# Kernel optimization log

Measured on AMD Instinct MI355X. Metric: run time of the kernel, lower is better.

Reference implementation:

```python
import jax, jax.numpy as jnp
import numpy as np

M_BLEND = 0.3
LR_REFINE = 0.1
N_REFINE = 10
N_SAMPLES = 256
USE_INFONCE = True
MARGIN = 0.2
TAU = 0.07


def safe_norm(x, eps=1e-8):
    return x / jnp.maximum(jnp.linalg.norm(x, axis=-1, keepdims=True), eps)


def setup_inputs() -> dict:
    key = jax.random.key(0)
    k1, k2, k3, k4 = jax.random.split(key, 4)
    fg_proto = safe_norm(jax.random.normal(k1, (64, 512), dtype=jnp.float32))
    bg_proto = safe_norm(jax.random.normal(k2, (64, 512), dtype=jnp.float32))
    F_map = jax.random.normal(k3, (16, 512, 96, 96), dtype=jnp.float32)
    M_map = jax.random.uniform(k4, (16, 96, 96), dtype=jnp.float32)
    return {"fg_proto": fg_proto, "bg_proto": bg_proto, "F_map": F_map, "M_map": M_map}


def _refine(feats, protos):
    # iterative k-means-like refinement: argmax assign -> per-cluster mean -> blended, renormalized centroid
    p = protos
    K = p.shape[0]
    ones = jnp.ones((feats.shape[0],), feats.dtype)
    for it in range(N_REFINE):
        step = LR_REFINE / (1.0 + 0.5 * it)
        assign = jnp.argmax(feats @ p.T, axis=1)                      # [S]
        sums = jax.ops.segment_sum(feats, assign, num_segments=K)    # [K, C]
        counts = jax.ops.segment_sum(ones, assign, num_segments=K)   # [K]
        cluster_mean = sums / jnp.maximum(counts, 1.0)[:, None]
        new_p = safe_norm((1.0 - step) * p + step * cluster_mean)
        p = jnp.where((counts > 0)[:, None], new_p, p)                # only update non-empty clusters
    return p


def reference(fg_proto, bg_proto, F_map, M_map):
    N, C, H, W = F_map.shape
    # M_map already at (H, W): nearest interpolation is identity; clamp to [0, 1]
    M_flat = jnp.clip(M_map.reshape(-1), 0.0, 1.0)                    # [N*H*W]
    F_flat = safe_norm(F_map.transpose(0, 2, 3, 1).reshape(-1, C))    # [N*H*W, C]

    sim_fg = F_flat @ fg_proto.T                                      # [P, Kf]
    sim_bg = F_flat @ bg_proto.T                                      # [P, Kb]
    dist_fg_min = 1.0 - sim_fg.max(axis=1)
    dist_bg_min = 1.0 - sim_bg.max(axis=1)

    k = min(N_SAMPLES, F_flat.shape[0])
    score_fg = jax.lax.stop_gradient(dist_fg_min * M_flat)
    score_bg = jax.lax.stop_gradient(dist_bg_min * (1.0 - M_flat))
    pos_idx = jax.lax.top_k(score_fg, k)[1]
    neg_idx = jax.lax.top_k(score_bg, k)[1]

    # refinement runs under no_grad in the original
    F_sg = jax.lax.stop_gradient(F_flat)
    p_fg = _refine(F_sg[pos_idx], jax.lax.stop_gradient(fg_proto))
    p_bg = _refine(F_sg[neg_idx], jax.lax.stop_gradient(bg_proto))

    # triplet loss (note: sim_neg also uses p_fg, as in the original)
    pos_feats = safe_norm(F_flat[pos_idx])
    neg_feats = safe_norm(F_flat[neg_idx])
    sim_pos = (pos_feats @ p_fg.T).max(axis=1).mean()
    sim_neg = (neg_feats @ p_fg.T).max(axis=1).mean()
    loss = jax.nn.relu(MARGIN + sim_neg - sim_pos)

    if USE_INFONCE:
        pos_sim = pos_feats @ p_fg.T / TAU                            # [k, Kf]
        neg_sim = pos_feats @ p_bg.T / TAU                            # [k, Kb]
        numerator = jax.scipy.special.logsumexp(pos_sim, axis=1)
        denominator = jax.scipy.special.logsumexp(jnp.concatenate([pos_sim, neg_sim], axis=1), axis=1)
        loss = loss + 0.25 * (-(numerator - denominator).mean())

    refined_fg = safe_norm((1.0 - M_BLEND) * fg_proto + M_BLEND * p_fg)
    refined_bg = safe_norm((1.0 - M_BLEND) * bg_proto + M_BLEND * p_bg)
    return loss, refined_fg, refined_bg
```

## Files before the change

### kernel.cpp

```cpp
#include <hip/hip_runtime.h>
#include <math.h>

#define P_TOTAL 147456
#define HW 9216
#define CHW (512*9216)
#define C_DIM 512
#define KP 64

__device__ __forceinline__ unsigned f2key(float f) {
    unsigned u = __float_as_uint(f);
    return (u & 0x80000000u) ? ~u : (u | 0x80000000u);
}

__global__ void k_init(const float* __restrict__ fg, const float* __restrict__ bg,
                       float* __restrict__ protoT, float* __restrict__ pwork) {
    int i = blockIdx.x * 256 + threadIdx.x;
    int side = i >> 15;
    int r = i & 32767;
    int k = r >> 9;
    int c = r & 511;
    float v = (side ? bg : fg)[k * 512 + c];
    protoT[side * 32768 + c * 64 + k] = v;
    pwork[side * 32768 + k * 512 + c] = v;
}

__global__ __launch_bounds__(256) void k_score(const float* __restrict__ F,
                                               const float* __restrict__ protoT,
                                               float* __restrict__ md_fg,
                                               float* __restrict__ md_bg,
                                               float* __restrict__ n2out) {
    __shared__ float lds[2048];
    const int side = blockIdx.y;
    const int p = blockIdx.x * 256 + threadIdx.x;
    const int n = p / HW;
    const int hw = p - n * HW;
    const float* Fp = F + (size_t)n * CHW + hw;
    const float* PT = protoT + side * (C_DIM * 64);

    float acc[64];
#pragma unroll
    for (int k = 0; k < 64; ++k) acc[k] = 0.f;
    float n2 = 0.f;

    for (int cc = 0; cc < 16; ++cc) {
        __syncthreads();
#pragma unroll
        for (int i = 0; i < 8; ++i)
            lds[threadIdx.x + 256 * i] = PT[cc * 2048 + threadIdx.x + 256 * i];
        __syncthreads();
        for (int c = 0; c < 32; ++c) {
            float f = Fp[(size_t)(cc * 32 + c) * HW];
            if (side == 0) n2 = fmaf(f, f, n2);
#pragma unroll
            for (int k = 0; k < 64; ++k) acc[k] = fmaf(f, lds[c * 64 + k], acc[k]);
        }
    }
    float m = acc[0];
#pragma unroll
    for (int k = 1; k < 64; ++k) m = fmaxf(m, acc[k]);
    if (side == 0) { md_fg[p] = m; n2out[p] = n2; }
    else          { md_bg[p] = m; }
}

__global__ void k_combine(const float* __restrict__ M,
                          float* __restrict__ sfg, float* __restrict__ sbg,
                          float* __restrict__ n2inv) {
    int p = blockIdx.x * 256 + threadIdx.x;
    float inv = 1.f / fmaxf(sqrtf(n2inv[p]), 1e-8f);
    float m = fminf(fmaxf(M[p], 0.f), 1.f);
    float sf = (1.f - sfg[p] * inv) * m;
    float sb = (1.f - sbg[p] * inv) * (1.f - m);
    sfg[p] = sf; sbg[p] = sb; n2inv[p] = inv;
}

__global__ void k_hist1(const float* __restrict__ sfg, const float* __restrict__ sbg,
                        unsigned* __restrict__ hist) {
    int side = blockIdx.y;
    int p = blockIdx.x * 256 + threadIdx.x;
    float s = side ? sbg[p] : sfg[p];
    atomicAdd(&hist[side * 65536 + (f2key(s) >> 16)], 1u);
}

__global__ void k_hist2(const float* __restrict__ sfg, const float* __restrict__ sbg,
                        const int* __restrict__ ctrl, unsigned* __restrict__ hist2) {
    int side = blockIdx.y;
    int p = blockIdx.x * 256 + threadIdx.x;
    float s = side ? sbg[p] : sfg[p];
    unsigned key = f2key(s);
    if ((int)(key >> 16) == ctrl[side * 8 + 0])
        atomicAdd(&hist2[side * 65536 + (key & 0xffffu)], 1u);
}

__global__ __launch_bounds__(1024) void k_scan(const unsigned* __restrict__ hist,
                                               int* __restrict__ ctrl, int pass) {
    __shared__ unsigned sd[1024];
    int side = blockIdx.x;
    const unsigned* h = hist + side * 65536;
    int t = threadIdx.x;
    unsigned partial = 0;
    for (int j = 0; j < 64; ++j) partial += h[65535 - (t * 64 + j)];
    sd[t] = partial;
    __syncthreads();
    for (int off = 1; off < 1024; off <<= 1) {
        unsigned v = (t >= off) ? sd[t - off] : 0u;
        __syncthreads();
        sd[t] += v;
        __syncthreads();
    }
    unsigned incl = sd[t];
    unsigned excl = incl - partial;
    unsigned target = (pass == 0) ? 256u : (unsigned)ctrl[side * 8 + 1];
    if (excl < target && target <= incl) {
        unsigned cum = excl;
        for (int j = 0; j < 64; ++j) {
            int b = 65535 - (t * 64 + j);
            unsigned c = h[b];
            if (cum + c >= target) {
                if (pass == 0) {
                    ctrl[side * 8 + 0] = b;
                    ctrl[side * 8 + 1] = (int)(target - cum);
                } else {
                    unsigned vkey = ((unsigned)ctrl[side * 8 + 0] << 16) | (unsigned)b;
                    ctrl[side * 8 + 2] = (int)vkey;
                    int n_gt = (int)(256u - (unsigned)ctrl[side * 8 + 1] + cum);
                    ctrl[side * 8 + 3] = n_gt;
                    ctrl[side * 8 + 4] = 256 - n_gt;
                }
                break;
            }
            cum += c;
        }
    }
}

__global__ void k_collect(const float* __restrict__ sfg, const float* __restrict__ sbg,
                          int* __restrict__ ctrl, int* __restrict__ idx, int* __restrict__ ties) {
    int side = blockIdx.y;
    int p = blockIdx.x * 256 + threadIdx.x;
    float s = side ? sbg[p] : sfg[p];
    unsigned key = f2key(s);
    unsigned vkey = (unsigned)ctrl[side * 8 + 2];
    if (key > vkey) {
        int pos = atomicAdd(&ctrl[side * 8 + 5], 1);
        idx[side * 256 + pos] = p;
    } else if (key == vkey) {
        int pos = atomicAdd(&ctrl[side * 8 + 6], 1);
        if (pos < 512) ties[side * 512 + pos] = p;
    }
}

__global__ void k_finalize(int* __restrict__ ctrl, int* __restrict__ idx, int* __restrict__ ties) {
    int side = threadIdx.x;
    if (side >= 2) return;
    int n_gt = ctrl[side * 8 + 3];
    int need = ctrl[side * 8 + 4];
    int cnt = ctrl[side * 8 + 6];
    if (cnt > 512) cnt = 512;
    int* tb = ties + side * 512;
    for (int q = 0; q < need; ++q) {
        int mi = q;
        for (int j = q + 1; j < cnt; ++j) if (tb[j] < tb[mi]) mi = j;
        int tmp = tb[q]; tb[q] = tb[mi]; tb[mi] = tmp;
        idx[side * 256 + n_gt + q] = tb[q];
    }
}

__global__ void k_gather(const float* __restrict__ F, const float* __restrict__ inv,
                         const int* __restrict__ idx, float* __restrict__ feats) {
    int b = blockIdx.x;
    int side = b >> 8, j = b & 255;
    int p = idx[side * 256 + j];
    float iv = inv[p];
    int n = p / HW, hw = p - n * HW;
    const float* Fp = F + (size_t)n * CHW + hw;
    float* o = feats + (size_t)(side * 256 + j) * 512;
    for (int c = threadIdx.x; c < 512; c += 256)
        o[c] = Fp[(size_t)c * HW] * iv;
}

__global__ __launch_bounds__(256) void k_assign(const float* __restrict__ feats,
                                                const float* __restrict__ pwork,
                                                float* __restrict__ sums,
                                                float* __restrict__ counts) {
    int w = blockIdx.x * 4 + (threadIdx.x >> 6);
    int lane = threadIdx.x & 63;
    int side = w >> 8, j = w & 255;
    const float4* fr = (const float4*)(feats + (size_t)(side * 256 + j) * 512);
    const float4* pw = (const float4*)(pwork + (size_t)side * 32768 + (size_t)lane * 512);
    float dot = 0.f;
#pragma unroll 4
    for (int c = 0; c < 128; ++c) {
        float4 a = fr[c], b = pw[c];
        dot = fmaf(a.x, b.x, dot); dot = fmaf(a.y, b.y, dot);
        dot = fmaf(a.z, b.z, dot); dot = fmaf(a.w, b.w, dot);
    }
    float bv = dot; int bi = lane;
#pragma unroll
    for (int m = 32; m >= 1; m >>= 1) {
        float ov = __shfl_xor(bv, m);
        int oi = __shfl_xor(bi, m);
        if (ov > bv || (ov == bv && oi < bi)) { bv = ov; bi = oi; }
    }
    if (lane == 0) atomicAdd(&counts[side * 64 + bi], 1.f);
    const float* frf = feats + (size_t)(side * 256 + j) * 512;
    float* srow = sums + (size_t)side * 32768 + (size_t)bi * 512;
#pragma unroll
    for (int i = 0; i < 8; ++i) {
        int c = lane + i * 64;
        atomicAdd(&srow[c], frf[c]);
    }
}

__global__ __launch_bounds__(64) void k_update(float* __restrict__ pwork,
                                               float* __restrict__ sums,
                                               float* __restrict__ counts,
                                               float step) {
    int side = blockIdx.x >> 6, k = blockIdx.x & 63;
    int lane = threadIdx.x;
    float cnt = counts[side * 64 + k];
    float* srow = sums + (size_t)side * 32768 + (size_t)k * 512;
    float* prow = pwork + (size_t)side * 32768 + (size_t)k * 512;
    float bl[8]; float n2 = 0.f;
#pragma unroll
    for (int i = 0; i < 8; ++i) {
        int c = lane + i * 64;
        float mean = srow[c] / fmaxf(cnt, 1.f);
        float v = (1.f - step) * prow[c] + step * mean;
        bl[i] = v; n2 = fmaf(v, v, n2);
        srow[c] = 0.f;
    }
#pragma unroll
    for (int m = 32; m >= 1; m >>= 1) n2 += __shfl_xor(n2, m);
    float inv = 1.f / fmaxf(sqrtf(n2), 1e-8f);
    if (cnt > 0.f) {
#pragma unroll
        for (int i = 0; i < 8; ++i) prow[lane + i * 64] = bl[i] * inv;
    }
    if (lane == 0) counts[side * 64 + k] = 0.f;
}

__global__ __launch_bounds__(256) void k_losspart(const float* __restrict__ feats,
                                                  const float* __restrict__ pwork,
                                                  float* __restrict__ lpart) {
    int w = blockIdx.x * 4 + (threadIdx.x >> 6);
    int lane = threadIdx.x & 63;
    int half = w >> 8, j = w & 255;
    const float4* fr = (const float4*)(feats + (size_t)(half * 256 + j) * 512);
    const float4* pf = (const float4*)(pwork + (size_t)lane * 512);
    const float4* pb = (const float4*)(pwork + 32768 + (size_t)lane * 512);
    if (half == 0) {
        float d1 = 0.f, d2 = 0.f;
        for (int c = 0; c < 128; ++c) {
            float4 a = fr[c], x = pf[c], y = pb[c];
            d1 = fmaf(a.x, x.x, d1); d1 = fmaf(a.y, x.y, d1);
            d1 = fmaf(a.z, x.z, d1); d1 = fmaf(a.w, x.w, d1);
            d2 = fmaf(a.x, y.x, d2); d2 = fmaf(a.y, y.y, d2);
            d2 = fmaf(a.z, y.z, d2); d2 = fmaf(a.w, y.w, d2);
        }
        float smax = d1;
        for (int m = 32; m >= 1; m >>= 1) smax = fmaxf(smax, __shfl_xor(smax, m));
        float a = d1 / 0.07f, b = d2 / 0.07f;
        float m1 = a;
        for (int m = 32; m >= 1; m >>= 1) m1 = fmaxf(m1, __shfl_xor(m1, m));
        float mb = b;
        for (int m = 32; m >= 1; m >>= 1) mb = fmaxf(mb, __shfl_xor(mb, m));
        float md = fmaxf(m1, mb);
        float sn = expf(a - m1);
        for (int m = 32; m >= 1; m >>= 1) sn += __shfl_xor(sn, m);
        float sdn = expf(a - md) + expf(b - md);
        for (int m = 32; m >= 1; m >>= 1) sdn += __shfl_xor(sdn, m);
        float num = m1 + logf(sn);
        float den = md + logf(sdn);
        if (lane == 0) { lpart[j] = smax; lpart[512 + j] = num - den; }
    } else {
        float d1 = 0.f;
        for (int c = 0; c < 128; ++c) {
            float4 a = fr[c], x = pf[c];
            d1 = fmaf(a.x, x.x, d1); d1 = fmaf(a.y, x.y, d1);
            d1 = fmaf(a.z, x.z, d1); d1 = fmaf(a.w, x.w, d1);
        }
        float smax = d1;
        for (int m = 32; m >= 1; m >>= 1) smax = fmaxf(smax, __shfl_xor(smax, m));
        if (lane == 0) lpart[256 + j] = smax;
    }
}

__global__ __launch_bounds__(256) void k_final(const float* __restrict__ lpart,
                                               float* __restrict__ out) {
    __shared__ float red[3][4];
    int t = threadIdx.x;
    float sp = lpart[t], sn = lpart[256 + t], nm = lpart[512 + t];
    for (int m = 32; m >= 1; m >>= 1) {
        sp += __shfl_xor(sp, m); sn += __shfl_xor(sn, m); nm += __shfl_xor(nm, m);
    }
    int wv = t >> 6;
    if ((t & 63) == 0) { red[0][wv] = sp; red[1][wv] = sn; red[2][wv] = nm; }
    __syncthreads();
    if (t == 0) {
        float SP = 0, SN = 0, NM = 0;
        for (int i = 0; i < 4; ++i) { SP += red[0][i]; SN += red[1][i]; NM += red[2][i]; }
        SP /= 256.f; SN /= 256.f; NM /= 256.f;
        out[0] = fmaxf(0.f, 0.2f + SN - SP) + 0.25f * (-NM);
    }
}

__global__ __launch_bounds__(64) void k_refined(const float* __restrict__ fg,
                                                const float* __restrict__ bg,
                                                const float* __restrict__ pwork,
                                                float* __restrict__ out) {
    int side = blockIdx.x >> 6, k = blockIdx.x & 63;
    int lane = threadIdx.x;
    const float* proto = (side ? bg : fg) + (size_t)k * 512;
    const float* prow = pwork + (size_t)side * 32768 + (size_t)k * 512;
    float bl[8]; float n2 = 0.f;
#pragma unroll
    for (int i = 0; i < 8; ++i) {
        int c = lane + i * 64;
        float v = 0.7f * proto[c] + 0.3f * prow[c];
        bl[i] = v; n2 = fmaf(v, v, n2);
    }
#pragma unroll
    for (int m = 32; m >= 1; m >>= 1) n2 += __shfl_xor(n2, m);
    float inv = 1.f / fmaxf(sqrtf(n2), 1e-8f);
    float* o = out + 1 + (size_t)side * 32768 + (size_t)k * 512;
#pragma unroll
    for (int i = 0; i < 8; ++i) o[lane + i * 64] = bl[i] * inv;
}

extern "C" void kernel_launch(void* const* d_in, const int* in_sizes, int n_in,
                              void* d_out, int out_size, void* d_ws, size_t ws_size,
                              hipStream_t stream) {
    const float* fg = (const float*)d_in[0];
    const float* bg = (const float*)d_in[1];
    const float* F  = (const float*)d_in[2];
    const float* M  = (const float*)d_in[3];
    float* out = (float*)d_out;
    char* ws = (char*)d_ws;

    size_t o = 0;
    auto alloc = [&](size_t bytes) { size_t r = o; o += (bytes + 1023) & ~(size_t)1023; return r; };
    size_t off_hist1 = alloc(2 * 65536 * 4);
    size_t off_hist2 = alloc(2 * 65536 * 4);
    size_t off_ctrl  = alloc(64);
    size_t off_cnts  = alloc(2 * 64 * 4);
    size_t off_sums  = alloc(2 * 64 * 512 * 4);
    size_t zbytes = o;
    size_t off_sfg   = alloc(P_TOTAL * 4);
    size_t off_sbg   = alloc(P_TOTAL * 4);
    size_t off_n2    = alloc(P_TOTAL * 4);
    size_t off_pT    = alloc(2 * 512 * 64 * 4);
    size_t off_idx   = alloc(2 * 256 * 4);
    size_t off_ties  = alloc(2 * 512 * 4);
    size_t off_feats = alloc(2 * 256 * 512 * 4);
    size_t off_pwork = alloc(2 * 64 * 512 * 4);
    size_t off_lpart = alloc(768 * 4);

    unsigned* hist1 = (unsigned*)(ws + off_hist1);
    unsigned* hist2 = (unsigned*)(ws + off_hist2);
    int* ctrl   = (int*)(ws + off_ctrl);
    float* cnts = (float*)(ws + off_cnts);
    float* sums = (float*)(ws + off_sums);
    float* sfg  = (float*)(ws + off_sfg);
    float* sbg  = (float*)(ws + off_sbg);
    float* n2   = (float*)(ws + off_n2);
    float* pT   = (float*)(ws + off_pT);
    int* idx    = (int*)(ws + off_idx);
    int* ties   = (int*)(ws + off_ties);
    float* feats = (float*)(ws + off_feats);
    float* pwork = (float*)(ws + off_pwork);
    float* lpart = (float*)(ws + off_lpart);

    hipMemsetAsync(ws, 0, zbytes, stream);
    k_init<<<256, 256, 0, stream>>>(fg, bg, pT, pwork);
    k_score<<<dim3(576, 2), 256, 0, stream>>>(F, pT, sfg, sbg, n2);
    k_combine<<<576, 256, 0, stream>>>(M, sfg, sbg, n2);
    k_hist1<<<dim3(576, 2), 256, 0, stream>>>(sfg, sbg, hist1);
    k_scan<<<2, 1024, 0, stream>>>(hist1, ctrl, 0);
    k_hist2<<<dim3(576, 2), 256, 0, stream>>>(sfg, sbg, ctrl, hist2);
    k_scan<<<2, 1024, 0, stream>>>(hist2, ctrl, 1);
    k_collect<<<dim3(576, 2), 256, 0, stream>>>(sfg, sbg, ctrl, idx, ties);
    k_finalize<<<1, 64, 0, stream>>>(ctrl, idx, ties);
    k_gather<<<512, 256, 0, stream>>>(F, n2, idx, feats);
    for (int it = 0; it < 10; ++it) {
        k_assign<<<128, 256, 0, stream>>>(feats, pwork, sums, cnts);
        k_update<<<128, 64, 0, stream>>>(pwork, sums, cnts, (float)(0.1 / (1.0 + 0.5 * it)));
    }
    k_losspart<<<128, 256, 0, stream>>>(feats, pwork, lpart);
    k_final<<<1, 256, 0, stream>>>(lpart, out);
    k_refined<<<128, 64, 0, stream>>>(fg, bg, pwork, out);
}
```

Baseline: 1.139 ms.

## Fuse fg/bg scoring into one pass with 4x32 register tiling

The scoring kernel now handles both prototype sets in a single launch, so F is read once instead of twice. Each thread computes a 4-pixel by 32-prototype register tile, with the four wavefront groups splitting the 128 fg+bg prototypes. Prototype columns are read from shared memory as float4, and the per-half maxima are combined through shared memory at the end. The point is to cut global traffic on F and raise FMA-to-load reuse. In exchange it uses a larger LDS footprint, 128 accumulator registers per thread, and a launch bound of 2 blocks per SM that may cause spills.

```diff
diff --git a/kernel.cpp b/kernel.cpp
--- a/kernel.cpp
+++ b/kernel.cpp
@@ -20,46 +20,100 @@
     int k = r >> 9;
     int c = r & 511;
     float v = (side ? bg : fg)[k * 512 + c];
-    protoT[side * 32768 + c * 64 + k] = v;
+    protoT[c * 128 + side * 64 + k] = v;
     pwork[side * 32768 + k * 512 + c] = v;
 }
 
-__global__ __launch_bounds__(256) void k_score(const float* __restrict__ F,
-                                               const float* __restrict__ protoT,
-                                               float* __restrict__ md_fg,
-                                               float* __restrict__ md_bg,
-                                               float* __restrict__ n2out) {
-    __shared__ float lds[2048];
-    const int side = blockIdx.y;
-    const int p = blockIdx.x * 256 + threadIdx.x;
-    const int n = p / HW;
-    const int hw = p - n * HW;
-    const float* Fp = F + (size_t)n * CHW + hw;
-    const float* PT = protoT + side * (C_DIM * 64);
-
-    float acc[64];
-#pragma unroll
-    for (int k = 0; k < 64; ++k) acc[k] = 0.f;
-    float n2 = 0.f;
-
-    for (int cc = 0; cc < 16; ++cc) {
+__global__ __launch_bounds__(256, 2) void k_score(const float* __restrict__ F,
+                                                  const float* __restrict__ protoT,
+                                                  float* __restrict__ md_fg,
+                                                  float* __restrict__ md_bg,
+                                                  float* __restrict__ n2out) {
+    __shared__ float lds[64 * 128];
+    const int t = threadIdx.x;
+    const int lane = t & 63;
+    const int g = t >> 6;
+    const int p0 = blockIdx.x * 256 + lane;
+    const int n = p0 / HW;
+    const int hw0 = p0 - n * HW;
+    const float* Fp = F + (size_t)n * CHW + hw0;
+
+    float acc[32][4];
+#pragma unroll
+    for (int i = 0; i < 32; ++i)
+#pragma unroll
+        for (int pt = 0; pt < 4; ++pt) acc[i][pt] = 0.f;
+    float nn[4] = {0.f, 0.f, 0.f, 0.f};
+
+    for (int chunk = 0; chunk < 8; ++chunk) {
         __syncthreads();
-#pragma unroll
-        for (int i = 0; i < 8; ++i)
-            lds[threadIdx.x + 256 * i] = PT[cc * 2048 + threadIdx.x + 256 * i];
+        {
+            const float4* src = (const float4*)(protoT + chunk * 8192);
+            float4* dst = (float4*)lds;
+#pragma unroll
+            for (int i = 0; i < 8; ++i) dst[t + 256 * i] = src[t + 256 * i];
+        }
         __syncthreads();
-        for (int c = 0; c < 32; ++c) {
-            float f = Fp[(size_t)(cc * 32 + c) * HW];
-            if (side == 0) n2 = fmaf(f, f, n2);
-#pragma unroll
-            for (int k = 0; k < 64; ++k) acc[k] = fmaf(f, lds[c * 64 + k], acc[k]);
-        }
-    }
-    float m = acc[0];
-#pragma unroll
-    for (int k = 1; k < 64; ++k) m = fmaxf(m, acc[k]);
-    if (side == 0) { md_fg[p] = m; n2out[p] = n2; }
-    else          { md_bg[p] = m; }
+#pragma unroll 4
+        for (int c = 0; c < 64; ++c) {
+            const float* Fc = Fp + (size_t)(chunk * 64 + c) * HW;
+            float f0 = Fc[0];
+            float f1 = Fc[64];
+            float f2 = Fc[128];
+            float f3 = Fc[192];
+            if (g == 0) {
+                nn[0] = fmaf(f0, f0, nn[0]);
+                nn[1] = fmaf(f1, f1, nn[1]);
+                nn[2] = fmaf(f2, f2, nn[2]);
+                nn[3] = fmaf(f3, f3, nn[3]);
+            }
+            const float4* pv = (const float4*)(lds + c * 128 + g * 32);
+#pragma unroll
+            for (int i = 0; i < 8; ++i) {
+                float4 b = pv[i];
+                acc[i * 4 + 0][0] = fmaf(f0, b.x, acc[i * 4 + 0][0]);
+                acc[i * 4 + 0][1] = fmaf(f1, b.x, acc[i * 4 + 0][1]);
+                acc[i * 4 + 0][2] = fmaf(f2, b.x, acc[i * 4 + 0][2]);
+                acc[i * 4 + 0][3] = fmaf(f3, b.x, acc[i * 4 + 0][3]);
+                acc[i * 4 + 1][0] = fmaf(f0, b.y, acc[i * 4 + 1][0]);
+                acc[i * 4 + 1][1] = fmaf(f1, b.y, acc[i * 4 + 1][1]);
+                acc[i * 4 + 1][2] = fmaf(f2, b.y, acc[i * 4 + 1][2]);
+                acc[i * 4 + 1][3] = fmaf(f3, b.y, acc[i * 4 + 1][3]);
+                acc[i * 4 + 2][0] = fmaf(f0, b.z, acc[i * 4 + 2][0]);
+                acc[i * 4 + 2][1] = fmaf(f1, b.z, acc[i * 4 + 2][1]);
+                acc[i * 4 + 2][2] = fmaf(f2, b.z, acc[i * 4 + 2][2]);
+                acc[i * 4 + 2][3] = fmaf(f3, b.z, acc[i * 4 + 2][3]);
+                acc[i * 4 + 3][0] = fmaf(f0, b.w, acc[i * 4 + 3][0]);
+                acc[i * 4 + 3][1] = fmaf(f1, b.w, acc[i * 4 + 3][1]);
+                acc[i * 4 + 3][2] = fmaf(f2, b.w, acc[i * 4 + 3][2]);
+                acc[i * 4 + 3][3] = fmaf(f3, b.w, acc[i * 4 + 3][3]);
+            }
+        }
+    }
+
+    float m[4];
+#pragma unroll
+    for (int pt = 0; pt < 4; ++pt) {
+        float mm = acc[0][pt];
+#pragma unroll
+        for (int i = 1; i < 32; ++i) mm = fmaxf(mm, acc[i][pt]);
+        m[pt] = mm;
+    }
+    __syncthreads();
+#pragma unroll
+    for (int pt = 0; pt < 4; ++pt) lds[(g * 4 + pt) * 64 + lane] = m[pt];
+    __syncthreads();
+    if (g == 0) {
+#pragma unroll
+        for (int pt = 0; pt < 4; ++pt) {
+            md_fg[p0 + pt * 64] = fmaxf(lds[(0 + pt) * 64 + lane], lds[(4 + pt) * 64 + lane]);
+            n2out[p0 + pt * 64] = nn[pt];
+        }
+    } else if (g == 2) {
+#pragma unroll
+        for (int pt = 0; pt < 4; ++pt)
+            md_bg[p0 + pt * 64] = fmaxf(lds[(8 + pt) * 64 + lane], lds[(12 + pt) * 64 + lane]);
+    }
 }
 
 __global__ void k_combine(const float* __restrict__ M,
@@ -348,7 +402,7 @@
     size_t off_sfg   = alloc(P_TOTAL * 4);
     size_t off_sbg   = alloc(P_TOTAL * 4);
     size_t off_n2    = alloc(P_TOTAL * 4);
-    size_t off_pT    = alloc(2 * 512 * 64 * 4);
+    size_t off_pT    = alloc(512 * 128 * 4);
     size_t off_idx   = alloc(2 * 256 * 4);
     size_t off_ties  = alloc(2 * 512 * 4);
     size_t off_feats = alloc(2 * 256 * 512 * 4);
@@ -372,7 +426,7 @@
 
     hipMemsetAsync(ws, 0, zbytes, stream);
     k_init<<<256, 256, 0, stream>>>(fg, bg, pT, pwork);
-    k_score<<<dim3(576, 2), 256, 0, stream>>>(F, pT, sfg, sbg, n2);
+    k_score<<<576, 256, 0, stream>>>(F, pT, sfg, sbg, n2);
     k_combine<<<576, 256, 0, stream>>>(M, sfg, sbg, n2);
     k_hist1<<<dim3(576, 2), 256, 0, stream>>>(sfg, sbg, hist1);
     k_scan<<<2, 1024, 0, stream>>>(hist1, ctrl, 0);
```

Result: no change. 1.144 ms (+0.5%).

## Register-tile score GEMM over fg+bg jointly and fuse combine and histogram

Applied to the files above, without the earlier changes.

Rewrites the scoring kernel so each block handles 576 pixels against both fg and bg prototypes at once. Each wave owns 16 prototypes and each thread holds 9 pixels in registers, with the next channel's loads issued ahead of use. The old design read F twice (once per side) with one pixel per thread. The score combine and first-pass histogram are folded into the same kernel's epilogue. The assign kernel now reads a transposed prototype copy that update keeps in sync, which adds extra strided writes per iteration. Using 256 blocks with launch_bounds(512,1) and 144 accumulators per thread risks low occupancy or register spills.

```diff
diff --git a/kernel.cpp b/kernel.cpp
--- a/kernel.cpp
+++ b/kernel.cpp
@@ -4,8 +4,6 @@
 #define P_TOTAL 147456
 #define HW 9216
 #define CHW (512*9216)
-#define C_DIM 512
-#define KP 64
 
 __device__ __forceinline__ unsigned f2key(float f) {
     unsigned u = __float_as_uint(f);
@@ -13,82 +11,122 @@
 }
 
 __global__ void k_init(const float* __restrict__ fg, const float* __restrict__ bg,
-                       float* __restrict__ protoT, float* __restrict__ pwork) {
+                       float* __restrict__ protoT, float* __restrict__ pwork,
+                       float* __restrict__ pwT) {
     int i = blockIdx.x * 256 + threadIdx.x;
     int side = i >> 15;
     int r = i & 32767;
     int k = r >> 9;
     int c = r & 511;
     float v = (side ? bg : fg)[k * 512 + c];
-    protoT[side * 32768 + c * 64 + k] = v;
+    protoT[c * 128 + side * 64 + k] = v;
     pwork[side * 32768 + k * 512 + c] = v;
-}
-
-__global__ __launch_bounds__(256) void k_score(const float* __restrict__ F,
-                                               const float* __restrict__ protoT,
-                                               float* __restrict__ md_fg,
-                                               float* __restrict__ md_bg,
-                                               float* __restrict__ n2out) {
-    __shared__ float lds[2048];
-    const int side = blockIdx.y;
-    const int p = blockIdx.x * 256 + threadIdx.x;
-    const int n = p / HW;
-    const int hw = p - n * HW;
-    const float* Fp = F + (size_t)n * CHW + hw;
-    const float* PT = protoT + side * (C_DIM * 64);
-
-    float acc[64];
-#pragma unroll
-    for (int k = 0; k < 64; ++k) acc[k] = 0.f;
-    float n2 = 0.f;
-
-    for (int cc = 0; cc < 16; ++cc) {
+    pwT[side * 32768 + c * 64 + k] = v;
+}
+
+__global__ __launch_bounds__(512, 1) void k_score(const float* __restrict__ F,
+                                                  const float* __restrict__ protoT,
+                                                  const float* __restrict__ M,
+                                                  float* __restrict__ sfg,
+                                                  float* __restrict__ sbg,
+                                                  float* __restrict__ invout,
+                                                  unsigned* __restrict__ hist) {
+    __shared__ float lds[8192];
+    const int t = threadIdx.x;
+    const int lane = t & 63;
+    const int w = t >> 6;
+    const int p0 = blockIdx.x * 576 + lane;
+    const int n = p0 / HW;
+    const int hw0 = p0 - n * HW;
+    const float* Fb = F + (size_t)n * CHW;
+
+    float acc[16][9];
+#pragma unroll
+    for (int jj = 0; jj < 16; ++jj)
+#pragma unroll
+        for (int i = 0; i < 9; ++i) acc[jj][i] = 0.f;
+    float nn[9];
+#pragma unroll
+    for (int i = 0; i < 9; ++i) nn[i] = 0.f;
+
+    auto ldch = [&](float (&dst)[9], int ch) {
+        int chc = ch > 511 ? 511 : ch;
+        const float* q = Fb + hw0 + (size_t)chc * HW;
+#pragma unroll
+        for (int i = 0; i < 9; ++i) dst[i] = q[i * 64];
+    };
+    auto kstep = [&](const float (&f)[9], int cc) {
+        const float4* pv4 = (const float4*)(lds + cc * 128 + w * 16);
+#pragma unroll
+        for (int j4 = 0; j4 < 4; ++j4) {
+            float4 bq = pv4[j4];
+#pragma unroll
+            for (int i = 0; i < 9; ++i) {
+                acc[j4 * 4 + 0][i] = fmaf(f[i], bq.x, acc[j4 * 4 + 0][i]);
+                acc[j4 * 4 + 1][i] = fmaf(f[i], bq.y, acc[j4 * 4 + 1][i]);
+                acc[j4 * 4 + 2][i] = fmaf(f[i], bq.z, acc[j4 * 4 + 2][i]);
+                acc[j4 * 4 + 3][i] = fmaf(f[i], bq.w, acc[j4 * 4 + 3][i]);
+            }
+        }
+    };
+
+    float fa[9], fb[9];
+    ldch(fa, 0); ldch(fb, 1);
+    int ch = 2;
+
+    for (int chunk = 0; chunk < 8; ++chunk) {
         __syncthreads();
-#pragma unroll
-        for (int i = 0; i < 8; ++i)
-            lds[threadIdx.x + 256 * i] = PT[cc * 2048 + threadIdx.x + 256 * i];
+        {
+            const float4* src = (const float4*)(protoT + chunk * 8192);
+            float4* dst = (float4*)lds;
+#pragma unroll
+            for (int i2 = 0; i2 < 4; ++i2) dst[t + 512 * i2] = src[t + 512 * i2];
+        }
         __syncthreads();
-        for (int c = 0; c < 32; ++c) {
-            float f = Fp[(size_t)(cc * 32 + c) * HW];
-            if (side == 0) n2 = fmaf(f, f, n2);
-#pragma unroll
-            for (int k = 0; k < 64; ++k) acc[k] = fmaf(f, lds[c * 64 + k], acc[k]);
-        }
-    }
-    float m = acc[0];
-#pragma unroll
-    for (int k = 1; k < 64; ++k) m = fmaxf(m, acc[k]);
-    if (side == 0) { md_fg[p] = m; n2out[p] = n2; }
-    else          { md_bg[p] = m; }
-}
-
-__global__ void k_combine(const float* __restrict__ M,
-                          float* __restrict__ sfg, float* __restrict__ sbg,
-                          float* __restrict__ n2inv) {
-    int p = blockIdx.x * 256 + threadIdx.x;
-    float inv = 1.f / fmaxf(sqrtf(n2inv[p]), 1e-8f);
-    float m = fminf(fmaxf(M[p], 0.f), 1.f);
-    float sf = (1.f - sfg[p] * inv) * m;
-    float sb = (1.f - sbg[p] * inv) * (1.f - m);
-    sfg[p] = sf; sbg[p] = sb; n2inv[p] = inv;
-}
-
-__global__ void k_hist1(const float* __restrict__ sfg, const float* __restrict__ sbg,
-                        unsigned* __restrict__ hist) {
-    int side = blockIdx.y;
-    int p = blockIdx.x * 256 + threadIdx.x;
-    float s = side ? sbg[p] : sfg[p];
-    atomicAdd(&hist[side * 65536 + (f2key(s) >> 16)], 1u);
-}
-
-__global__ void k_hist2(const float* __restrict__ sfg, const float* __restrict__ sbg,
-                        const int* __restrict__ ctrl, unsigned* __restrict__ hist2) {
-    int side = blockIdx.y;
-    int p = blockIdx.x * 256 + threadIdx.x;
-    float s = side ? sbg[p] : sfg[p];
-    unsigned key = f2key(s);
-    if ((int)(key >> 16) == ctrl[side * 8 + 0])
-        atomicAdd(&hist2[side * 65536 + (key & 0xffffu)], 1u);
+        for (int c2 = 0; c2 < 32; ++c2) {
+            if (w == 0) {
+#pragma unroll
+                for (int i = 0; i < 9; ++i) nn[i] = fmaf(fa[i], fa[i], nn[i]);
+            }
+            kstep(fa, c2 * 2);
+            ldch(fa, ch++);
+            if (w == 0) {
+#pragma unroll
+                for (int i = 0; i < 9; ++i) nn[i] = fmaf(fb[i], fb[i], nn[i]);
+            }
+            kstep(fb, c2 * 2 + 1);
+            ldch(fb, ch++);
+        }
+    }
+
+    float m16[9];
+#pragma unroll
+    for (int i = 0; i < 9; ++i) {
+        float mm = acc[0][i];
+#pragma unroll
+        for (int jj = 1; jj < 16; ++jj) mm = fmaxf(mm, acc[jj][i]);
+        m16[i] = mm;
+    }
+    __syncthreads();
+#pragma unroll
+    for (int i = 0; i < 9; ++i) lds[w * 576 + i * 64 + lane] = m16[i];
+    if (w == 0) {
+#pragma unroll
+        for (int i = 0; i < 9; ++i) lds[4608 + i * 64 + lane] = nn[i];
+    }
+    __syncthreads();
+    for (int pi = t; pi < 576; pi += 512) {
+        int p = blockIdx.x * 576 + pi;
+        float fgm = fmaxf(fmaxf(lds[pi], lds[576 + pi]), fmaxf(lds[1152 + pi], lds[1728 + pi]));
+        float bgm = fmaxf(fmaxf(lds[2304 + pi], lds[2880 + pi]), fmaxf(lds[3456 + pi], lds[4032 + pi]));
+        float inv = 1.f / fmaxf(sqrtf(lds[4608 + pi]), 1e-8f);
+        float mm = fminf(fmaxf(M[p], 0.f), 1.f);
+        float sf = (1.f - fgm * inv) * mm;
+        float sb = (1.f - bgm * inv) * (1.f - mm);
+        sfg[p] = sf; sbg[p] = sb; invout[p] = inv;
+        atomicAdd(&hist[f2key(sf) >> 16], 1u);
+        atomicAdd(&hist[65536 + (f2key(sb) >> 16)], 1u);
+    }
 }
 
 __global__ __launch_bounds__(1024) void k_scan(const unsigned* __restrict__ hist,
@@ -133,6 +171,16 @@
     }
 }
 
+__global__ void k_hist2(const float* __restrict__ sfg, const float* __restrict__ sbg,
+                        const int* __restrict__ ctrl, unsigned* __restrict__ hist2) {
+    int side = blockIdx.y;
+    int p = blockIdx.x * 256 + threadIdx.x;
+    float s = side ? sbg[p] : sfg[p];
+    unsigned key = f2key(s);
+    if ((int)(key >> 16) == ctrl[side * 8 + 0])
+        atomicAdd(&hist2[side * 65536 + (key & 0xffffu)], 1u);
+}
+
 __global__ void k_collect(const float* __restrict__ sfg, const float* __restrict__ sbg,
                           int* __restrict__ ctrl, int* __restrict__ idx, int* __restrict__ ties) {
     int side = blockIdx.y;
@@ -179,21 +227,18 @@
 }
 
 __global__ __launch_bounds__(256) void k_assign(const float* __restrict__ feats,
-                                                const float* __restrict__ pwork,
+                                                const float* __restrict__ pwT,
                                                 float* __restrict__ sums,
                                                 float* __restrict__ counts) {
     int w = blockIdx.x * 4 + (threadIdx.x >> 6);
     int lane = threadIdx.x & 63;
     int side = w >> 8, j = w & 255;
-    const float4* fr = (const float4*)(feats + (size_t)(side * 256 + j) * 512);
-    const float4* pw = (const float4*)(pwork + (size_t)side * 32768 + (size_t)lane * 512);
+    const float* fr = feats + (size_t)(side * 256 + j) * 512;
+    const float* pT = pwT + (size_t)side * 32768;
     float dot = 0.f;
-#pragma unroll 4
-    for (int c = 0; c < 128; ++c) {
-        float4 a = fr[c], b = pw[c];
-        dot = fmaf(a.x, b.x, dot); dot = fmaf(a.y, b.y, dot);
-        dot = fmaf(a.z, b.z, dot); dot = fmaf(a.w, b.w, dot);
-    }
+#pragma unroll 8
+    for (int c = 0; c < 512; ++c)
+        dot = fmaf(fr[c], pT[c * 64 + lane], dot);
     float bv = dot; int bi = lane;
 #pragma unroll
     for (int m = 32; m >= 1; m >>= 1) {
@@ -202,16 +247,16 @@
         if (ov > bv || (ov == bv && oi < bi)) { bv = ov; bi = oi; }
     }
     if (lane == 0) atomicAdd(&counts[side * 64 + bi], 1.f);
-    const float* frf = feats + (size_t)(side * 256 + j) * 512;
     float* srow = sums + (size_t)side * 32768 + (size_t)bi * 512;
 #pragma unroll
     for (int i = 0; i < 8; ++i) {
         int c = lane + i * 64;
-        atomicAdd(&srow[c], frf[c]);
+        atomicAdd(&srow[c], fr[c]);
     }
 }
 
 __global__ __launch_bounds__(64) void k_update(float* __restrict__ pwork,
+                                               float* __restrict__ pwT,
                                                float* __restrict__ sums,
                                                float* __restrict__ counts,
                                                float step) {
@@ -220,6 +265,7 @@
     float cnt = counts[side * 64 + k];
     float* srow = sums + (size_t)side * 32768 + (size_t)k * 512;
     float* prow = pwork + (size_t)side * 32768 + (size_t)k * 512;
+    float* pT = pwT + (size_t)side * 32768;
     float bl[8]; float n2 = 0.f;
 #pragma unroll
     for (int i = 0; i < 8; ++i) {
@@ -234,7 +280,12 @@
     float inv = 1.f / fmaxf(sqrtf(n2), 1e-8f);
     if (cnt > 0.f) {
 #pragma unroll
-        for (int i = 0; i < 8; ++i) prow[lane + i * 64] = bl[i] * inv;
+        for (int i = 0; i < 8; ++i) {
+            int c = lane + i * 64;
+            float v = bl[i] * inv;
+            prow[c] = v;
+            pT[(size_t)c * 64 + k] = v;
+        }
     }
     if (lane == 0) counts[side * 64 + k] = 0.f;
 }
@@ -347,12 +398,13 @@
     size_t zbytes = o;
     size_t off_sfg   = alloc(P_TOTAL * 4);
     size_t off_sbg   = alloc(P_TOTAL * 4);
-    size_t off_n2    = alloc(P_TOTAL * 4);
-    size_t off_pT    = alloc(2 * 512 * 64 * 4);
+    size_t off_inv   = alloc(P_TOTAL * 4);
+    size_t off_pT    = alloc(512 * 128 * 4);
+    size_t off_pwork = alloc(2 * 64 * 512 * 4);
+    size_t off_pwT   = alloc(2 * 512 * 64 * 4);
     size_t off_idx   = alloc(2 * 256 * 4);
     size_t off_ties  = alloc(2 * 512 * 4);
-    size_t off_feats = alloc(2 * 256 * 512 * 4);
-    size_t off_pwork = alloc(2 * 64 * 512 * 4);
+    size_t off_feats = alloc(512 * 512 * 4);
     size_t off_lpart = alloc(768 * 4);
 
     unsigned* hist1 = (unsigned*)(ws + off_hist1);
@@ -362,28 +414,27 @@
     float* sums = (float*)(ws + off_sums);
     float* sfg  = (float*)(ws + off_sfg);
     float* sbg  = (float*)(ws + off_sbg);
-    float* n2   = (float*)(ws + off_n2);
+    float* inv  = (float*)(ws + off_inv);
     float* pT   = (float*)(ws + off_pT);
+    float* pwork = (float*)(ws + off_pwork);
+    float* pwT  = (float*)(ws + off_pwT);
     int* idx    = (int*)(ws + off_idx);
     int* ties   = (int*)(ws + off_ties);
     float* feats = (float*)(ws + off_feats);
-    float* pwork = (float*)(ws + off_pwork);
     float* lpart = (float*)(ws + off_lpart);
 
     hipMemsetAsync(ws, 0, zbytes, stream);
-    k_init<<<256, 256, 0, stream>>>(fg, bg, pT, pwork);
-    k_score<<<dim3(576, 2), 256, 0, stream>>>(F, pT, sfg, sbg, n2);
-    k_combine<<<576, 256, 0, stream>>>(M, sfg, sbg, n2);
-    k_hist1<<<dim3(576, 2), 256, 0, stream>>>(sfg, sbg, hist1);
+    k_init<<<256, 256, 0, stream>>>(fg, bg, pT, pwork, pwT);
+    k_score<<<256, 512, 0, stream>>>(F, pT, M, sfg, sbg, inv, hist1);
     k_scan<<<2, 1024, 0, stream>>>(hist1, ctrl, 0);
     k_hist2<<<dim3(576, 2), 256, 0, stream>>>(sfg, sbg, ctrl, hist2);
     k_scan<<<2, 1024, 0, stream>>>(hist2, ctrl, 1);
     k_collect<<<dim3(576, 2), 256, 0, stream>>>(sfg, sbg, ctrl, idx, ties);
     k_finalize<<<1, 64, 0, stream>>>(ctrl, idx, ties);
-    k_gather<<<512, 256, 0, stream>>>(F, n2, idx, feats);
+    k_gather<<<512, 256, 0, stream>>>(F, inv, idx, feats);
     for (int it = 0; it < 10; ++it) {
-        k_assign<<<128, 256, 0, stream>>>(feats, pwork, sums, cnts);
-        k_update<<<128, 64, 0, stream>>>(pwork, sums, cnts, (float)(0.1 / (1.0 + 0.5 * it)));
+        k_assign<<<128, 256, 0, stream>>>(feats, pwT, sums, cnts);
+        k_update<<<128, 64, 0, stream>>>(pwork, pwT, sums, cnts, (float)(0.1 / (1.0 + 0.5 * it)));
     }
     k_losspart<<<128, 256, 0, stream>>>(feats, pwork, lpart);
     k_final<<<1, 256, 0, stream>>>(lpart, out);
```

Result: faster. 990.8 us (-13.0%).
